# Kernel tuning notes

Measured on AMD Instinct MI355X. Metric: run time of the kernel, lower is better.

Reference implementation:

```python
import jax, jax.numpy as jnp
import numpy as np
from jax import lax

B, T, D = 8, 704, 1024
R, K, HD = 16, 4, 64          # num_rules, top_k(rules), head_dim
SD, E = 32, 3                 # select_dim, num_entities
CTX = E // 2                  # entities kept per selected rule = 1
SEG_LENS = np.array([128.0, 64.0, 512.0], np.float32)  # prompt / descriptor / input segments
SEG_LENS_J = jnp.asarray(SEG_LENS)


def _seg_mask():
    m = np.zeros((E, T), np.float32)
    m[0, :128] = 1.0
    m[1, 128:192] = 1.0
    m[2, 192:] = 1.0
    return jnp.asarray(m)


def _ln(x, g, b):
    mu = x.mean(-1, keepdims=True)
    var = ((x - mu) ** 2).mean(-1, keepdims=True)
    return (x - mu) * lax.rsqrt(var + 1e-5) * g + b


def _st_topk(scores, k):
    # hard top-k multi-hot mask with straight-through gradient (TopkArgMax)
    _, idx = lax.top_k(scores, k)
    hard = jax.nn.one_hot(idx, scores.shape[-1], dtype=scores.dtype).sum(-2)
    return hard + scores - lax.stop_gradient(scores)


def setup_inputs() -> dict:
    key = jax.random.key(0)
    ks = jax.random.split(key, 16)
    g = lambda i, shape, s=0.02: jax.random.normal(ks[i], shape, jnp.float32) * s
    return dict(
        hidden_states=jax.random.normal(ks[0], (B, T, D), jnp.float32),
        attention_mask=jnp.zeros((B, T, T), jnp.float32),
        rules_embed=g(1, (K, R, HD), 0.1),
        W_ent=g(2, (D, SD)), b_ent=jnp.zeros((SD,), jnp.float32),
        Wq_er=g(3, (HD, SD)), Wk_er=g(4, (SD, SD)),
        Wq_es=g(5, (K, HD, SD // 2)), Wk_es=g(6, (SD, SD // 2)),
        Wq=g(7, (D, D)), bq=jnp.zeros((D,), jnp.float32),
        Wk=g(8, (D, D)), bk=jnp.zeros((D,), jnp.float32),
        Wv=g(9, (D, D)), bv=jnp.zeros((D,), jnp.float32),
        Wo=g(10, (HD, D)), bo=jnp.zeros((D,), jnp.float32),
        ln1_g=jnp.ones((D,), jnp.float32), ln1_b=jnp.zeros((D,), jnp.float32),
        ln2_g=jnp.ones((D,), jnp.float32), ln2_b=jnp.zeros((D,), jnp.float32),
        fc1_w1=g(11, (D, D // 2)), fc1_w2=g(12, (D // 2, 4 * D)),
        fc2_w1=g(13, (4 * D, D // 2)), fc2_w2=g(14, (D // 2, D)),
    )


def _forward(hidden_states, attention_mask, rules_embed, W_ent, b_ent,
             Wq_er, Wk_er, Wq_es, Wk_es, Wq, bq, Wk, bk, Wv, bv, Wo, bo,
             ln1_g, ln1_b, ln2_g, ln2_b, fc1_w1, fc1_w2, fc2_w1, fc2_w2):
    seg = _seg_mask()                                   # [E,T] entity token masks
    residual = hidden_states
    h = _ln(hidden_states, ln1_g, ln1_b)                # [B,T,D]

    # --- EntityEncoder: masked mean-pool per entity segment -> select_dim
    pooled = jnp.einsum('et,btd->bed', seg, h) / SEG_LENS_J[None, :, None]
    entities = pooled @ W_ent + b_ent                   # [B,E,SD]

    # --- rule/entity selection (eval: hard top-1 over rules x entities)
    q_er = jnp.einsum('krh,hd->krd', rules_embed, Wq_er)           # [K,R,SD] shared query
    k_er = entities @ Wk_er                                        # [B,E,SD]
    s_er = jnp.einsum('krd,bed->bkre', q_er, k_er) / np.float32(np.sqrt(SD))
    mask = _st_topk(s_er.reshape(B, K, R * E), 1)                  # [B,K,R*E]
    rule_mask = mask.reshape(B, K, R, E).sum(-1)                   # [B,K,R]
    selected_rules = jnp.einsum('bkr,krh->bkh', rule_mask, rules_embed)  # [B,K,HD]

    # --- entity selection per selected rule (grouped query, top-ctx_size)
    q_es = jnp.einsum('bkh,khi->bki', selected_rules, Wq_es)
    k_es = entities @ Wk_es                                        # [B,E,SD//2]
    s_es = jnp.einsum('bki,bei->bke', q_es, k_es) / np.float32(np.sqrt(SD // 2))
    entity_mask = _st_topk(s_es, CTX)                              # [B,K,E]

    # --- masked gather-sum over (top_k, entities) without [B,K,E,T,D] blowup
    tok_gate = jnp.einsum('bke,et->bt', entity_mask, seg)          # [B,T]
    hg = h * tok_gate[:, :, None]                                  # [B,T,D]

    # --- per-rule self-attention
    scale = np.float32(HD ** -0.5)
    q = ((hg @ Wq + bq) * scale).reshape(B, T, R, HD).transpose(0, 2, 1, 3)
    kk = (hg @ Wk + bk).reshape(B, T, R, HD).transpose(0, 2, 1, 3)
    v = (hg @ Wv + bv).reshape(B, T, R, HD).transpose(0, 2, 1, 3)
    aw = jnp.einsum('brqh,brkh->brqk', q, kk) + attention_mask[:, None]
    ap = jax.nn.softmax(aw, axis=-1)
    ao = jnp.einsum('brqk,brkh->brqh', ap, v)                      # [B,R,T,HD]

    # --- combine over rules per top-k slot, project, sum over slots
    sel = jnp.einsum('bkr,brth->bkth', rule_mask, ao)              # [B,K,T,HD]
    attn_out = (jnp.einsum('bkth,hd->bktd', sel, Wo) + bo).sum(1)  # [B,T,D] (bias summed K times, as in torch)

    h = residual + attn_out
    residual = h
    x = _ln(h, ln2_g, ln2_b).reshape(B * T, D)
    # GroupMLP (num=1, hidden=D//2) with internal relu; outer activation_fn=gelu
    x = jax.nn.gelu(jax.nn.relu(x @ fc1_w1) @ fc1_w2, approximate=False)
    x = jax.nn.relu(x @ fc2_w1) @ fc2_w2
    return residual + x.reshape(B, T, D)


def reference(hidden_states, attention_mask, rules_embed, W_ent, b_ent,
              Wq_er, Wk_er, Wq_es, Wk_es, Wq, bq, Wk, bk, Wv, bv, Wo, bo,
              ln1_g, ln1_b, ln2_g, ln2_b, fc1_w1, fc1_w2, fc2_w1, fc2_w2):
    return _forward(hidden_states, attention_mask, rules_embed, W_ent, b_ent,
                    Wq_er, Wk_er, Wq_es, Wk_es, Wq, bq, Wk, bk, Wv, bv, Wo, bo,
                    ln1_g, ln1_b, ln2_g, ln2_b, fc1_w1, fc1_w2, fc2_w1, fc2_w2)
```

## Files before the change

kernel.cpp:

```cpp
#include <hip/hip_runtime.h>
#include <hip/hip_bf16.h>
#include <math.h>

#define BB 8
#define TT 704
#define DD 1024
#define RR 16
#define KK 4
#define HDH 64
#define BT (BB*TT)

typedef unsigned short u16;
typedef __attribute__((ext_vector_type(4))) float f32x4;
typedef __attribute__((ext_vector_type(8))) short bf16x8;
typedef __attribute__((ext_vector_type(4))) unsigned short u16x4;
typedef __attribute__((ext_vector_type(8))) unsigned short u16x8;

__device__ __forceinline__ u16 f2bf(float f) {
    union { float f; unsigned int u; } cv; cv.f = f;
    unsigned int u = cv.u;
    unsigned int r = (u + 0x7fffu + ((u >> 16) & 1u)) >> 16;
    return (u16)r;
}

__device__ __forceinline__ float bf2f(u16 v) {
    union { unsigned int u; float f; } cv; cv.u = ((unsigned int)v) << 16;
    return cv.f;
}

__device__ __forceinline__ void gl2lds(const u16* g, u16* l) {
    __builtin_amdgcn_global_load_lds(
        (const __attribute__((address_space(1))) void*)g,
        (__attribute__((address_space(3))) void*)l, 16, 0, 0);
}

template<int N> __device__ __forceinline__ void waitv() {
    if constexpr (N == 0) asm volatile("s_waitcnt vmcnt(0)" ::: "memory");
    else if constexpr (N == 2) asm volatile("s_waitcnt vmcnt(2)" ::: "memory");
    else if constexpr (N == 3) asm volatile("s_waitcnt vmcnt(3)" ::: "memory");
    else asm volatile("s_waitcnt vmcnt(4)" ::: "memory");
}

__device__ __forceinline__ int xcd_swz(int d, int nwg) {
    return (d & 7) * (nwg >> 3) + (d >> 3);
}

template<int OBF16, int IBF16>
__global__ __launch_bounds__(256)
void ln_kernel(const void* __restrict__ xv, const float* __restrict__ g,
               const float* __restrict__ be, void* __restrict__ yv)
{
    const int row = blockIdx.x;
    const int tid = threadIdx.x;
    __shared__ float sbuf[4];
    const size_t off = (size_t)row * DD + tid * 4;
    float4 v;
    if (IBF16) {
        u16x4 xb = *(const u16x4*)((const u16*)xv + off);
        v.x = bf2f(xb[0]); v.y = bf2f(xb[1]); v.z = bf2f(xb[2]); v.w = bf2f(xb[3]);
    } else {
        v = *(const float4*)((const float*)xv + off);
    }
    float s = v.x + v.y + v.z + v.w;
#pragma unroll
    for (int o = 32; o; o >>= 1) s += __shfl_xor(s, o);
    if ((tid & 63) == 0) sbuf[tid >> 6] = s;
    __syncthreads();
    float mean = (sbuf[0] + sbuf[1] + sbuf[2] + sbuf[3]) * (1.f / 1024.f);
    float dx = v.x - mean, dy = v.y - mean, dz = v.z - mean, dw = v.w - mean;
    float q = dx*dx + dy*dy + dz*dz + dw*dw;
    __syncthreads();
#pragma unroll
    for (int o = 32; o; o >>= 1) q += __shfl_xor(q, o);
    if ((tid & 63) == 0) sbuf[tid >> 6] = q;
    __syncthreads();
    float var = (sbuf[0] + sbuf[1] + sbuf[2] + sbuf[3]) * (1.f / 1024.f);
    float rstd = rsqrtf(var + 1e-5f);
    float4 gg = *(const float4*)(g + tid * 4);
    float4 bb4 = *(const float4*)(be + tid * 4);
    float o0 = dx * rstd * gg.x + bb4.x;
    float o1 = dy * rstd * gg.y + bb4.y;
    float o2 = dz * rstd * gg.z + bb4.z;
    float o3 = dw * rstd * gg.w + bb4.w;
    if (OBF16) {
        u16x4 o4 = {f2bf(o0), f2bf(o1), f2bf(o2), f2bf(o3)};
        *(u16x4*)((u16*)yv + off) = o4;
    } else {
        float4 o4 = {o0, o1, o2, o3};
        *(float4*)((float*)yv + off) = o4;
    }
}

__global__ __launch_bounds__(256)
void ln1_dual_kernel(const float* __restrict__ x, const float* __restrict__ g,
                     const float* __restrict__ be, float* __restrict__ y,
                     u16* __restrict__ yb)
{
    const int row = blockIdx.x;
    const int tid = threadIdx.x;
    __shared__ float sbuf[4];
    const size_t off = (size_t)row * DD + tid * 4;
    float4 v = *(const float4*)(x + off);
    float s = v.x + v.y + v.z + v.w;
#pragma unroll
    for (int o = 32; o; o >>= 1) s += __shfl_xor(s, o);
    if ((tid & 63) == 0) sbuf[tid >> 6] = s;
    __syncthreads();
    float mean = (sbuf[0] + sbuf[1] + sbuf[2] + sbuf[3]) * (1.f / 1024.f);
    float dx = v.x - mean, dy = v.y - mean, dz = v.z - mean, dw = v.w - mean;
    float q = dx*dx + dy*dy + dz*dz + dw*dw;
    __syncthreads();
#pragma unroll
    for (int o = 32; o; o >>= 1) q += __shfl_xor(q, o);
    if ((tid & 63) == 0) sbuf[tid >> 6] = q;
    __syncthreads();
    float var = (sbuf[0] + sbuf[1] + sbuf[2] + sbuf[3]) * (1.f / 1024.f);
    float rstd = rsqrtf(var + 1e-5f);
    float4 gg = *(const float4*)(g + tid * 4);
    float4 bb4 = *(const float4*)(be + tid * 4);
    float o0 = dx * rstd * gg.x + bb4.x;
    float o1 = dy * rstd * gg.y + bb4.y;
    float o2 = dz * rstd * gg.z + bb4.z;
    float o3 = dw * rstd * gg.w + bb4.w;
    float4 o4 = {o0, o1, o2, o3};
    *(float4*)(y + off) = o4;
    u16x4 ob = {f2bf(o0), f2bf(o1), f2bf(o2), f2bf(o3)};
    *(u16x4*)(yb + off) = ob;
}

__global__ __launch_bounds__(256)
void pool_partial_kernel(const float* __restrict__ h, float* __restrict__ partial)
{
    const int chunk = blockIdx.x, b = blockIdx.y;
    const int d = threadIdx.x * 4;
    const float* p = h + ((size_t)b * TT + chunk * 64) * DD + d;
    float4 s = {0.f, 0.f, 0.f, 0.f};
    for (int t = 0; t < 64; ++t) {
        float4 v = *(const float4*)(p + (size_t)t * DD);
        s.x += v.x; s.y += v.y; s.z += v.z; s.w += v.w;
    }
    *(float4*)(partial + ((size_t)(b * 11 + chunk)) * 1024 + d) = s;
}

__global__ __launch_bounds__(256)
void pool_finish_kernel(const float* __restrict__ partial, const float* __restrict__ W_ent,
                        const float* __restrict__ b_ent, float* __restrict__ entities)
{
    const int b = blockIdx.x / 3, e = blockIdx.x % 3;
    const int c0 = (e == 0) ? 0 : (e == 1) ? 2 : 3;
    const int c1 = (e == 0) ? 2 : (e == 1) ? 3 : 11;
    const float invlen = (e == 0) ? (1.f/128.f) : (e == 1) ? (1.f/64.f) : (1.f/512.f);
    __shared__ float pooled[1024];
    __shared__ float part[8][32];
    const int tid = threadIdx.x;
    {
        const int d = tid * 4;
        float4 s = {0.f, 0.f, 0.f, 0.f};
        for (int c = c0; c < c1; ++c) {
            float4 v = *(const float4*)(partial + ((size_t)(b * 11 + c)) * 1024 + d);
            s.x += v.x; s.y += v.y; s.z += v.z; s.w += v.w;
        }
        pooled[d+0] = s.x * invlen; pooled[d+1] = s.y * invlen;
        pooled[d+2] = s.z * invlen; pooled[d+3] = s.w * invlen;
    }
    __syncthreads();
    const int g = tid >> 5, j = tid & 31;
    float s = 0.f;
    for (int d = g * 128; d < g * 128 + 128; ++d) s = fmaf(pooled[d], W_ent[d * 32 + j], s);
    part[g][j] = s;
    __syncthreads();
    if (tid < 32) {
        float s2 = b_ent[tid];
        for (int g2 = 0; g2 < 8; ++g2) s2 += part[g2][tid];
        entities[blockIdx.x * 32 + tid] = s2;
    }
}

__global__ __launch_bounds__(256)
void select_kernel(const float* __restrict__ entities, const float* __restrict__ rules,
                   const float* __restrict__ Wq_er, const float* __restrict__ Wk_er,
                   const float* __restrict__ Wq_es, const float* __restrict__ Wk_es,
                   int* __restrict__ slot_rule, float* __restrict__ gate)
{
    __shared__ float rules_s[4096];
    __shared__ float Wq_er_s[2048];
    __shared__ float Wq_es_s[4096];
    __shared__ float Wk_er_s[1024];
    __shared__ float Wk_es_s[512];
    __shared__ float ent_s[768];
    __shared__ float q_er_s[2048];
    __shared__ float k_er_s[768];
    __shared__ float k_es_s[384];
    __shared__ float qes_s[32][16];
    __shared__ int   rsel_s[32];
    __shared__ int   sel_e[32];
    const int tid = threadIdx.x;
    for (int i = tid; i < 1024; i += 256) *(float4*)&rules_s[i*4] = *(const float4*)&rules[i*4];
    for (int i = tid; i < 512;  i += 256) *(float4*)&Wq_er_s[i*4] = *(const float4*)&Wq_er[i*4];
    for (int i = tid; i < 1024; i += 256) *(float4*)&Wq_es_s[i*4] = *(const float4*)&Wq_es[i*4];
    if (tid < 256) *(float4*)&Wk_er_s[tid*4] = *(const float4*)&Wk_er[tid*4];
    if (tid < 128) *(float4*)&Wk_es_s[tid*4] = *(const float4*)&Wk_es[tid*4];
    if (tid < 192) *(float4*)&ent_s[tid*4] = *(const float4*)&entities[tid*4];
    __syncthreads();
    for (int idx = tid; idx < 2048; idx += 256) {
        int k = idx >> 9, rem = idx & 511, r = rem >> 5, d = rem & 31;
        float s = 0.f;
        for (int hh = 0; hh < 64; ++hh)
            s = fmaf(rules_s[(k * 16 + r) * 64 + hh], Wq_er_s[hh * 32 + d], s);
        q_er_s[idx] = s;
    }
    for (int idx = tid; idx < 768; idx += 256) {
        int be = idx >> 5, d = idx & 31;
        float s = 0.f;
        for (int ss = 0; ss < 32; ++ss)
            s = fmaf(ent_s[be * 32 + ss], Wk_er_s[ss * 32 + d], s);
        k_er_s[idx] = s;
    }
    for (int idx = tid; idx < 384; idx += 256) {
        int be = idx >> 4, i = idx & 15;
        float s = 0.f;
        for (int ss = 0; ss < 32; ++ss)
            s = fmaf(ent_s[be * 32 + ss], Wk_es_s[ss * 16 + i], s);
        k_es_s[idx] = s;
    }
    __syncthreads();
    {
        const int pair = tid >> 3, slice = tid & 7;
        const int b = pair >> 2, k = pair & 3;
        float best = -1e30f; int bj = 48;
        for (int j = slice * 6; j < slice * 6 + 6; ++j) {
            const int r = j / 3, e = j - 3 * r;
            const float* qp = &q_er_s[(k * 16 + r) * 32];
            const float* kp = &k_er_s[(b * 3 + e) * 32];
            float s = 0.f;
            for (int d = 0; d < 32; ++d) s = fmaf(qp[d], kp[d], s);
            s *= 0.17677669529663687f;
            if (s > best) { best = s; bj = j; }
        }
#pragma unroll
        for (int off = 1; off < 8; off <<= 1) {
            float os = __shfl_xor(best, off);
            int oj = __shfl_xor(bj, off);
            if (os > best || (os == best && oj < bj)) { best = os; bj = oj; }
        }
        if (slice == 0) { rsel_s[pair] = bj / 3; slot_rule[pair] = bj / 3; }
    }
    __syncthreads();
    {
        const int pair = tid >> 3, slice = tid & 7;
        const int k = pair & 3, rstar = rsel_s[pair];
#pragma unroll
        for (int ii = 0; ii < 2; ++ii) {
            const int i = slice * 2 + ii;
            float s = 0.f;
            for (int hh = 0; hh < 64; ++hh)
                s = fmaf(rules_s[(k * 16 + rstar) * 64 + hh], Wq_es_s[(k * 64 + hh) * 16 + i], s);
            qes_s[pair][i] = s;
        }
    }
    __syncthreads();
    if ((tid & 7) == 0) {
        const int pair = tid >> 3, b = pair >> 2;
        float best2 = -1e30f; int ei = 0;
        for (int e = 0; e < 3; ++e) {
            float s = 0.f;
            for (int i = 0; i < 16; ++i) s = fmaf(qes_s[pair][i], k_es_s[(b * 3 + e) * 16 + i], s);
            s *= 0.25f;
            if (s > best2) { best2 = s; ei = e; }
        }
        sel_e[pair] = ei;
    }
    __syncthreads();
    if (tid < 24) {
        const int b = tid / 3, e = tid % 3;
        float g = 0.f;
        for (int k = 0; k < 4; ++k) g += (sel_e[b * 4 + k] == e) ? 1.f : 0.f;
        gate[b * 3 + e] = g;
    }
}

__device__ __forceinline__ void transpose_tile(const float* __restrict__ in,
                                               u16* __restrict__ out,
                                               int R, int C, int tr, int tc)
{
    __shared__ float tile[32][33];
    const int tx = threadIdx.x & 31, ty = threadIdx.x >> 5;
    const int c0 = tc * 32, r0 = tr * 32;
#pragma unroll
    for (int j = 0; j < 4; ++j)
        tile[ty + j * 8][tx] = in[(size_t)(r0 + ty + j * 8) * C + c0 + tx];
    __syncthreads();
#pragma unroll
    for (int j = 0; j < 4; ++j)
        out[(size_t)(c0 + ty + j * 8) * R + r0 + tx] = f2bf(tile[tx][ty + j * 8]);
}

__device__ __forceinline__ void transpose_tile_rep4(const float* __restrict__ in,
                                                    u16* __restrict__ out,
                                                    int tr, int tc)
{
    __shared__ float tile[32][33];
    const int tx = threadIdx.x & 31, ty = threadIdx.x >> 5;
    const int c0 = tc * 32, r0 = tr * 32;
#pragma unroll
    for (int j = 0; j < 4; ++j)
        tile[ty + j * 8][tx] = in[(size_t)(r0 + ty + j * 8) * 1024 + c0 + tx];
    __syncthreads();
#pragma unroll
    for (int j = 0; j < 4; ++j) {
        const u16 v = f2bf(tile[tx][ty + j * 8]);
        u16* o = out + (size_t)(c0 + ty + j * 8) * 256 + r0 + tx;
#pragma unroll
        for (int rep = 0; rep < 4; ++rep) o[rep * 64] = v;
    }
}

__global__ __launch_bounds__(256)
void transpose_batch1_kernel(const float* __restrict__ Wq, const float* __restrict__ Wk,
                             const float* __restrict__ Wv, const float* __restrict__ Wo,
                             const float* __restrict__ fc1w1, const float* __restrict__ fc2w2,
                             u16* __restrict__ WqkvT, u16* __restrict__ WoT4,
                             u16* __restrict__ fc1w1T, u16* __restrict__ fc2w2T)
{
    const int bid = blockIdx.x;
    if (bid < 3072) {
        const int m = bid >> 10, t = bid & 1023;
        const float* in = (m == 0) ? Wq : (m == 1) ? Wk : Wv;
        transpose_tile(in, WqkvT + (size_t)m * 1024 * 1024, 1024, 1024, t >> 5, t & 31);
    } else if (bid < 3136) {
        const int t = bid - 3072;
        transpose_tile_rep4(Wo, WoT4, t >> 5, t & 31);
    } else if (bid < 3648) {
        const int t = bid - 3136;
        transpose_tile(fc1w1, fc1w1T, 1024, 512, t >> 4, t & 15);
    } else {
        const int t = bid - 3648;
        transpose_tile(fc2w2, fc2w2T, 512, 1024, t >> 5, t & 31);
    }
}

__global__ __launch_bounds__(256)
void transpose_batch2_kernel(const float* __restrict__ fc1w2, const float* __restrict__ fc2w1,
                             u16* __restrict__ fc1w2T, u16* __restrict__ fc2w1T)
{
    const int bid = blockIdx.x;
    if (bid < 2048) transpose_tile(fc1w2, fc1w2T, 512, 4096, bid >> 7, bid & 127);
    else { const int t = bid - 2048; transpose_tile(fc2w1, fc2w1T, 4096, 512, t >> 4, t & 15); }
}

template<int BN, int ACT, int OBF16, int RESB, int SWZ>
__global__ __launch_bounds__(256)
void gemm2(const u16* __restrict__ A, int lda, const u16* __restrict__ Bt, int ldb,
           void* C0, void* C1, int ldc, int M, int Ksub,
           const void* __restrict__ resid, const float* __restrict__ bias, float bscale,
           int gx, int gy)
{
    constexpr int MI = (BN == 128) ? 4 : 2;
    constexpr int NLOAD = 2 + ((BN == 128) ? 2 : 1);
    __shared__ u16 As[3][128 * 32];
    __shared__ u16 Bs[3][BN * 32];
    const int tid = threadIdx.x;
    const int wid = tid >> 6, lane = tid & 63;
    const int bid = SWZ ? xcd_swz(blockIdx.x, gridDim.x) : (int)blockIdx.x;
    const int col = bid % gx;
    const int rem = bid / gx;
    const int row = rem % gy;
    const int z = rem / gy;
    const int row0 = row * 128, col0 = col * BN;
    const size_t koff = (size_t)z * Ksub;
    const int srA = wid * 32 + (lane >> 2);
    const int sc = (lane & 3) * 8;
    const u16* ag = A + (size_t)(row0 + srA) * lda + koff + sc;
    const int srB = (BN == 128) ? (wid * 32 + (lane >> 2)) : (wid * 16 + (lane >> 2));
    const u16* bg = Bt + (size_t)(col0 + srB) * ldb + koff + sc;
    const int nt = Ksub >> 5;

    auto STAGE = [&](int buf, int t) {
        const u16* a = ag + t * 32;
        const u16* b = bg + t * 32;
        gl2lds(a, &As[buf][wid * 1024]);
        gl2lds(a + (size_t)16 * lda, &As[buf][wid * 1024 + 512]);
        if constexpr (BN == 128) {
            gl2lds(b, &Bs[buf][wid * 1024]);
            gl2lds(b + (size_t)16 * ldb, &Bs[buf][wid * 1024 + 512]);
        } else {
            gl2lds(b, &Bs[buf][wid * 512]);
        }
    };

    f32x4 acc[MI][4];
#pragma unroll
    for (int i = 0; i < MI; ++i)
#pragma unroll
        for (int j = 0; j < 4; ++j) acc[i][j] = (f32x4){0.f, 0.f, 0.f, 0.f};

    const int fr = lane & 15, kb8 = (lane >> 4) * 8;
    const int wrbase = (BN == 128) ? (wid >> 1) * 64 : wid * 32;
    const int wcbase = (BN == 128) ? (wid & 1) * 64 : 0;
    const int paoff = (wrbase + fr) * 32 + kb8;
    const int pboff = (wcbase + fr) * 32 + kb8;

    STAGE(0, 0);
    if (nt > 1) STAGE(1, 1);
    for (int t = 0; t < nt; ++t) {
        if (t + 1 < nt) waitv<NLOAD>(); else waitv<0>();
        __builtin_amdgcn_s_barrier();
        asm volatile("" ::: "memory");
        const int buf = t % 3;
#pragma unroll
        for (int mi = 0; mi < MI; ++mi) {
            bf16x8 af = *(const bf16x8*)&As[buf][paoff + mi * 512];
#pragma unroll
            for (int ni = 0; ni < 4; ++ni) {
                bf16x8 bfv = *(const bf16x8*)&Bs[buf][pboff + ni * 512];
                acc[mi][ni] = __builtin_amdgcn_mfma_f32_16x16x32_bf16(af, bfv, acc[mi][ni], 0, 0, 0);
            }
        }
        if (t + 2 < nt) STAGE((t + 2) % 3, t + 2);
    }

    void* Cp = (z == 0) ? C0 : C1;
    const int fq4 = (lane >> 4) * 4;
#pragma unroll
    for (int mi = 0; mi < MI; ++mi) {
#pragma unroll
        for (int j = 0; j < 4; ++j) {
            const int rw = row0 + wrbase + mi * 16 + fq4 + j;
#pragma unroll
            for (int ni = 0; ni < 4; ++ni) {
                const int cl = col0 + wcbase + ni * 16 + fr;
                float v = acc[mi][ni][j];
                if (bias) v += bscale * bias[cl];
                if (ACT == 1) v = fmaxf(v, 0.f);
                else if (ACT == 2) v = 0.5f * v * (1.f + erff(v * 0.70710678118654752f));
                const size_t off = (size_t)rw * ldc + cl;
                if (OBF16) {
                    ((u16*)Cp)[off] = f2bf(v);
                } else {
                    if (resid) v += RESB ? bf2f(((const u16*)resid)[off])
                                         : ((const float*)resid)[off];
                    ((float*)Cp)[off] = v;
                }
            }
        }
    }
}

template<int NP>
__global__ __launch_bounds__(256)
void red_relu_kernel(const float* __restrict__ p0, const float* __restrict__ p1,
                     const float* __restrict__ p2, const float* __restrict__ p3,
                     u16* __restrict__ out)
{
    const int i = (blockIdx.x * 256 + threadIdx.x) * 4;
    float4 a = *(const float4*)(p0 + i);
    float4 b = *(const float4*)(p1 + i);
    a.x += b.x; a.y += b.y; a.z += b.z; a.w += b.w;
    if (NP == 4) {
        float4 c = *(const float4*)(p2 + i);
        float4 d = *(const float4*)(p3 + i);
        a.x += c.x + d.x; a.y += c.y + d.y; a.z += c.z + d.z; a.w += c.w + d.w;
    }
    u16x4 o = {f2bf(fmaxf(a.x, 0.f)), f2bf(fmaxf(a.y, 0.f)),
               f2bf(fmaxf(a.z, 0.f)), f2bf(fmaxf(a.w, 0.f))};
    *(u16x4*)(out + i) = o;
}

__global__ __launch_bounds__(256)
void combine_mfma_kernel(const u16* __restrict__ AO, const u16* __restrict__ WoT4,
                         const float* __restrict__ hidden, const float* __restrict__ bo,
                         u16* __restrict__ hmid)
{
    __shared__ u16 As[3][128 * 32];
    __shared__ u16 Bs[3][128 * 32];
    const int tid = threadIdx.x;
    const int wid = tid >> 6, lane = tid & 63;
    const int bid = xcd_swz(blockIdx.x, gridDim.x);
    const int row0 = (bid >> 3) * 128, col0 = (bid & 7) * 128;
    const int srA = wid * 32 + (lane >> 2);
    const int sc = (lane & 3) * 8;
    const int arow0 = row0 + srA, arow1 = arow0 + 16;
    const int ab0 = arow0 / TT, at0 = arow0 - ab0 * TT;
    const int ab1 = arow1 / TT, at1 = arow1 - ab1 * TT;
    const u16* abase0 = AO + ((size_t)(ab0 * 4) * TT + at0) * 64 + sc;
    const u16* abase1 = AO + ((size_t)(ab1 * 4) * TT + at1) * 64 + sc;
    const u16* bg = WoT4 + (size_t)(col0 + srA) * 256 + sc;
    const int nt = 8;

    auto STAGE = [&](int buf, int t) {
        const int k0 = t * 32;
        const size_t delta = (size_t)(k0 >> 6) * (TT * 64) + (k0 & 63);
        gl2lds(abase0 + delta, &As[buf][wid * 1024]);
        gl2lds(abase1 + delta, &As[buf][wid * 1024 + 512]);
        gl2lds(bg + k0, &Bs[buf][wid * 1024]);
        gl2lds(bg + k0 + (size_t)16 * 256, &Bs[buf][wid * 1024 + 512]);
    };

    f32x4 acc[4][4];
#pragma unroll
    for (int i = 0; i < 4; ++i)
#pragma unroll
        for (int j = 0; j < 4; ++j) acc[i][j] = (f32x4){0.f, 0.f, 0.f, 0.f};
    const int fr = lane & 15, kb8 = (lane >> 4) * 8;
    const int wrbase = (wid >> 1) * 64, wcbase = (wid & 1) * 64;
    const int paoff = (wrbase + fr) * 32 + kb8;
    const int pboff = (wcbase + fr) * 32 + kb8;

    STAGE(0, 0);
    STAGE(1, 1);
    for (int t = 0; t < nt; ++t) {
        if (t + 1 < nt) waitv<4>(); else waitv<0>();
        __builtin_amdgcn_s_barrier();
        asm volatile("" ::: "memory");
        const int buf = t % 3;
#pragma unroll
        for (int mi = 0; mi < 4; ++mi) {
            bf16x8 af = *(const bf16x8*)&As[buf][paoff + mi * 512];
#pragma unroll
            for (int ni = 0; ni < 4; ++ni) {
                bf16x8 bfv = *(const bf16x8*)&Bs[buf][pboff + ni * 512];
                acc[mi][ni] = __builtin_amdgcn_mfma_f32_16x16x32_bf16(af, bfv, acc[mi][ni], 0, 0, 0);
            }
        }
        if (t + 2 < nt) STAGE((t + 2) % 3, t + 2);
    }

    const int fq4 = (lane >> 4) * 4;
#pragma unroll
    for (int mi = 0; mi < 4; ++mi)
#pragma unroll
        for (int j = 0; j < 4; ++j) {
            const int rw = row0 + wrbase + mi * 16 + fq4 + j;
#pragma unroll
            for (int ni = 0; ni < 4; ++ni) {
                const int cl = col0 + wcbase + ni * 16 + fr;
                const size_t off = (size_t)rw * DD + cl;
                float v = acc[mi][ni][j] + 4.f * bo[cl] + hidden[off];
                hmid[off] = f2bf(v);
            }
        }
}

__global__ __launch_bounds__(256)
void qkv3_mfma_kernel(const u16* __restrict__ hb, const u16* __restrict__ WqkvT,
                      const float* __restrict__ bq, const float* __restrict__ bk,
                      const float* __restrict__ bv, const int* __restrict__ slot_rule,
                      const float* __restrict__ gatep,
                      u16* __restrict__ Qb, u16* __restrict__ Kb, u16* __restrict__ VT)
{
    const int bid = xcd_swz(blockIdx.x, gridDim.x);
    const int slot = bid & 3;
    const int mt = (bid >> 2) % 11;
    const int b = (bid >> 2) / 11;
    const int z = b * 4 + slot;
    const int r = slot_rule[z];
    const float gv = gatep[b * 3 + ((mt < 2) ? 0 : (mt < 3) ? 1 : 2)];
    __shared__ u16 As[3][64 * 32];
    __shared__ u16 Bs[3][3][64 * 32];
    const int tid = threadIdx.x;
    const int w = tid >> 6, lane = tid & 63;
    const u16* ag = hb + ((size_t)b * TT + mt * 64 + (tid >> 2)) * DD + (tid & 3) * 8;
    const u16* bg0 = WqkvT + (size_t)0 * DD * DD + (size_t)(r * 64 + (tid >> 2)) * DD + (tid & 3) * 8;
    const u16* bg1 = WqkvT + (size_t)1 * DD * DD + (size_t)(r * 64 + (tid >> 2)) * DD + (tid & 3) * 8;
    const u16* bg2 = WqkvT + (size_t)2 * DD * DD + (size_t)(r * 64 + (tid >> 2)) * DD + (tid & 3) * 8;
    auto STAGE = [&](int buf, int t) {
        gl2lds(ag  + t * 32, &As[buf][w * 512]);
        gl2lds(bg0 + t * 32, &Bs[buf][0][w * 512]);
        gl2lds(bg1 + t * 32, &Bs[buf][1][w * 512]);
        gl2lds(bg2 + t * 32, &Bs[buf][2][w * 512]);
    };
    f32x4 accq[4], acck[4], accv[4];
#pragma unroll
    for (int i = 0; i < 4; ++i) {
        accq[i] = (f32x4){0.f, 0.f, 0.f, 0.f};
        acck[i] = (f32x4){0.f, 0.f, 0.f, 0.f};
        accv[i] = (f32x4){0.f, 0.f, 0.f, 0.f};
    }
    const int fr = lane & 15, kb8 = (lane >> 4) * 8;
    const int paoff = (w * 16 + fr) * 32 + kb8;
    const int nt = 32;
    STAGE(0, 0);
    STAGE(1, 1);
    for (int t = 0; t < nt; ++t) {
        if (t + 1 < nt) waitv<4>(); else waitv<0>();
        __builtin_amdgcn_s_barrier();
        asm volatile("" ::: "memory");
        const int buf = t % 3;
        bf16x8 af = *(const bf16x8*)&As[buf][paoff];
#pragma unroll
        for (int ni = 0; ni < 4; ++ni) {
            const int boff = (ni * 16 + fr) * 32 + kb8;
            bf16x8 bq8 = *(const bf16x8*)&Bs[buf][0][boff];
            bf16x8 bk8 = *(const bf16x8*)&Bs[buf][1][boff];
            bf16x8 bv8 = *(const bf16x8*)&Bs[buf][2][boff];
            accq[ni] = __builtin_amdgcn_mfma_f32_16x16x32_bf16(af, bq8, accq[ni], 0, 0, 0);
            acck[ni] = __builtin_amdgcn_mfma_f32_16x16x32_bf16(af, bk8, acck[ni], 0, 0, 0);
            accv[ni] = __builtin_amdgcn_mfma_f32_16x16x32_bf16(bv8, af, accv[ni], 0, 0, 0);
        }
        if (t + 2 < nt) STAGE((t + 2) % 3, t + 2);
    }
    const size_t bs = (size_t)z * TT;
    const int fq4 = (lane >> 4) * 4;
#pragma unroll
    for (int ni = 0; ni < 4; ++ni)
#pragma unroll
        for (int j = 0; j < 4; ++j) {
            const int row = mt * 64 + w * 16 + fq4 + j;
            const int col = ni * 16 + fr;
            Qb[(bs + row) * 64 + col] = f2bf((gv * accq[ni][j] + bq[r * 64 + col]) * 0.125f);
            Kb[(bs + row) * 64 + col] = f2bf(gv * acck[ni][j] + bk[r * 64 + col]);
            const int d = ni * 16 + fq4 + j;
            const int tt2 = mt * 64 + w * 16 + fr;
            VT[((size_t)z * 64 + d) * TT + tt2] = f2bf(gv * accv[ni][j] + bv[r * 64 + d]);
        }
}

__global__ __launch_bounds__(256)
void attn_mfma_kernel(const u16* __restrict__ Qb, const u16* __restrict__ Kb,
                      const u16* __restrict__ VT, const float* __restrict__ amask,
                      u16* __restrict__ AO)
{
    const int bid = xcd_swz(blockIdx.x, gridDim.x);
    const int slot = bid & 3;
    const int qt = (bid >> 2) % 11;
    const int b = (bid >> 2) / 11;
    const int z = b * 4 + slot;
    const size_t bs = (size_t)z * TT;
    const int tid = threadIdx.x;
    const int w = tid >> 6, lane = tid & 63;
    const int fr = lane & 15, g = lane >> 4;
    const int q0 = qt * 64 + w * 16;

    __shared__ u16 Ks[64 * 72];
    __shared__ u16 VTs[64 * 72];
    __shared__ u16 Ps[4][16 * 72];

    bf16x8 qa[2];
    qa[0] = *(const bf16x8*)(Qb + (bs + q0 + fr) * 64 + g * 8);
    qa[1] = *(const bf16x8*)(Qb + (bs + q0 + fr) * 64 + 32 + g * 8);

    float m_run[4], l_run[4];
    f32x4 oacc[4];
#pragma unroll
    for (int j = 0; j < 4; ++j) { m_run[j] = -1e30f; l_run[j] = 0.f; }
#pragma unroll
    for (int ni = 0; ni < 4; ++ni) oacc[ni] = (f32x4){0.f, 0.f, 0.f, 0.f};

    const float* mrow = amask + ((size_t)b * TT + q0 + g * 4) * TT;

    for (int kc = 0; kc < 11; ++kc) {
        const int kv0 = kc * 64;
        __syncthreads();
#pragma unroll
        for (int it = 0; it < 2; ++it) {
            const int idx = tid + it * 256;
            const int row = idx >> 3, ch = (idx & 7) * 8;
            *(u16x8*)&Ks[row * 72 + ch]  = *(const u16x8*)(Kb + (bs + kv0 + row) * 64 + ch);
            *(u16x8*)&VTs[row * 72 + ch] = *(const u16x8*)(VT + ((size_t)z * 64 + row) * TT + kv0 + ch);
        }
        __syncthreads();
        f32x4 sacc[4];
#pragma unroll
        for (int ni = 0; ni < 4; ++ni) sacc[ni] = (f32x4){0.f, 0.f, 0.f, 0.f};
#pragma unroll
        for (int c = 0; c < 2; ++c)
#pragma unroll
            for (int ni = 0; ni < 4; ++ni) {
                bf16x8 bf = *(const bf16x8*)&Ks[(ni * 16 + fr) * 72 + c * 32 + g * 8];
                sacc[ni] = __builtin_amdgcn_mfma_f32_16x16x32_bf16(qa[c], bf, sacc[ni], 0, 0, 0);
            }
        float mloc[4] = {-1e30f, -1e30f, -1e30f, -1e30f};
#pragma unroll
        for (int ni = 0; ni < 4; ++ni)
#pragma unroll
            for (int j = 0; j < 4; ++j) {
                float s = sacc[ni][j] + mrow[(size_t)j * TT + kv0 + ni * 16 + fr];
                sacc[ni][j] = s;
                mloc[j] = fmaxf(mloc[j], s);
            }
#pragma unroll
        for (int o = 1; o < 16; o <<= 1)
#pragma unroll
            for (int j = 0; j < 4; ++j) mloc[j] = fmaxf(mloc[j], __shfl_xor(mloc[j], o));
        float fac[4], lsum[4];
#pragma unroll
        for (int j = 0; j < 4; ++j) {
            const float mn = fmaxf(m_run[j], mloc[j]);
            fac[j] = __expf(m_run[j] - mn);
            m_run[j] = mn;
            lsum[j] = 0.f;
        }
#pragma unroll
        for (int ni = 0; ni < 4; ++ni)
#pragma unroll
            for (int j = 0; j < 4; ++j) {
                const float p = __expf(sacc[ni][j] - m_run[j]);
                lsum[j] += p;
                Ps[w][(g * 4 + j) * 72 + ni * 16 + fr] = f2bf(p);
            }
#pragma unroll
        for (int o = 1; o < 16; o <<= 1)
#pragma unroll
            for (int j = 0; j < 4; ++j) lsum[j] += __shfl_xor(lsum[j], o);
#pragma unroll
        for (int j = 0; j < 4; ++j) l_run[j] = l_run[j] * fac[j] + lsum[j];
#pragma unroll
        for (int ni = 0; ni < 4; ++ni)
#pragma unroll
            for (int j = 0; j < 4; ++j) oacc[ni][j] *= fac[j];
#pragma unroll
        for (int c = 0; c < 2; ++c) {
            bf16x8 paf = *(const bf16x8*)&Ps[w][fr * 72 + c * 32 + g * 8];
#pragma unroll
            for (int ni = 0; ni < 4; ++ni) {
                bf16x8 vf = *(const bf16x8*)&VTs[(ni * 16 + fr) * 72 + c * 32 + g * 8];
                oacc[ni] = __builtin_amdgcn_mfma_f32_16x16x32_bf16(paf, vf, oacc[ni], 0, 0, 0);
            }
        }
    }
#pragma unroll
    for (int j = 0; j < 4; ++j) {
        const float inv = 1.f / l_run[j];
        const int t = q0 + g * 4 + j;
#pragma unroll
        for (int ni = 0; ni < 4; ++ni)
            AO[(bs + t) * 64 + ni * 16 + fr] = f2bf(oacc[ni][j] * inv);
    }
}

extern "C" void kernel_launch(void* const* d_in, const int* in_sizes, int n_in,
                              void* d_out, int out_size, void* d_ws, size_t ws_size,
                              hipStream_t stream)
{
    const float* hidden = (const float*)d_in[0];
    const float* amask  = (const float*)d_in[1];
    const float* rules  = (const float*)d_in[2];
    const float* W_ent  = (const float*)d_in[3];
    const float* b_ent  = (const float*)d_in[4];
    const float* Wq_er  = (const float*)d_in[5];
    const float* Wk_er  = (const float*)d_in[6];
    const float* Wq_es  = (const float*)d_in[7];
    const float* Wk_es  = (const float*)d_in[8];
    const float* Wq     = (const float*)d_in[9];
    const float* bq     = (const float*)d_in[10];
    const float* Wk     = (const float*)d_in[11];
    const float* bk     = (const float*)d_in[12];
    const float* Wv     = (const float*)d_in[13];
    const float* bv     = (const float*)d_in[14];
    const float* Wo     = (const float*)d_in[15];
    const float* bo     = (const float*)d_in[16];
    const float* ln1_g  = (const float*)d_in[17];
    const float* ln1_b  = (const float*)d_in[18];
    const float* ln2_g  = (const float*)d_in[19];
    const float* ln2_b  = (const float*)d_in[20];
    const float* fc1_w1 = (const float*)d_in[21];
    const float* fc1_w2 = (const float*)d_in[22];
    const float* fc2_w1 = (const float*)d_in[23];
    const float* fc2_w2 = (const float*)d_in[24];

    char* ws = (char*)d_ws;
    float* h      = (float*)(ws + 0);
    u16*   x1     = (u16*)(ws + 0);
    u16*   x3b    = (u16*)(ws + 5767168);
    float* g3p1   = (float*)(ws + 11534336);
    u16*   hmid   = (u16*)(ws + 23068672);
    u16*   hb     = (u16*)(ws + 46137344);
    u16*   xln2   = (u16*)(ws + 46137344);
    u16*   x2h    = (u16*)(ws + 46137344);
    u16*   Qb     = (u16*)(ws + 57671680);
    u16*   Kb     = (u16*)(ws + 60555264);
    u16*   VT     = (u16*)(ws + 66322432);
    u16*   AO     = (u16*)(ws + 69206016);
    float* part   = (float*)(ws + 69206016);
    float* g3p0   = (float*)(ws + 74973184);
    float* ent    = (float*)(ws + 80740352);
    float* gate   = (float*)(ws + 80743424);
    int*   srule  = (int*)(ws + 80743552);
    u16*   WqkvT  = (u16*)(ws + 80743680);
    u16*   fc1w2T = (u16*)(ws + 80743680);
    u16*   fc2w1T = (u16*)(ws + 84937984);
    u16*   WoT4   = (u16*)(ws + 89132288);
    u16*   fc1w1T = (u16*)(ws + 89656576);
    u16*   fc2w2T = (u16*)(ws + 90705152);
    float* out    = (float*)d_out;

    ln1_dual_kernel<<<BT, 256, 0, stream>>>(hidden, ln1_g, ln1_b, h, hb);
    pool_partial_kernel<<<dim3(11, 8), 256, 0, stream>>>(h, part);
    pool_finish_kernel<<<24, 256, 0, stream>>>(part, W_ent, b_ent, ent);
    select_kernel<<<1, 256, 0, stream>>>(ent, rules, Wq_er, Wk_er, Wq_es, Wk_es, srule, gate);

    transpose_batch1_kernel<<<4160, 256, 0, stream>>>(Wq, Wk, Wv, Wo, fc1_w1, fc2_w2,
                                                      WqkvT, WoT4, fc1w1T, fc2w2T);

    qkv3_mfma_kernel<<<352, 256, 0, stream>>>(hb, WqkvT, bq, bk, bv, srule, gate,
                                              Qb, Kb, VT);
    transpose_batch2_kernel<<<4096, 256, 0, stream>>>(fc1_w2, fc2_w1, fc1w2T, fc2w1T);

    attn_mfma_kernel<<<352, 256, 0, stream>>>(Qb, Kb, VT, amask, AO);

    combine_mfma_kernel<<<352, 256, 0, stream>>>(AO, WoT4, hidden, bo, hmid);

    ln_kernel<1, 1><<<BT, 256, 0, stream>>>(hmid, ln2_g, ln2_b, xln2);

    gemm2<64, 1, 1, 0, 1><<<352, 256, 0, stream>>>(
        xln2, 1024, fc1w1T, 1024, x1, nullptr, 512, BT, 1024,
        nullptr, nullptr, 0.f, 8, 44);

    for (int half = 0; half < 2; ++half) {
        const u16* x1h = x1 + (size_t)half * 2816 * 512;
        u16* x3bh = x3b + (size_t)half * 2816 * 512;
        gemm2<128, 2, 1, 0, 0><<<704, 256, 0, stream>>>(
            x1h, 512, fc1w2T, 512, x2h, nullptr, 4096, 2816, 512,
            nullptr, nullptr, 0.f, 32, 22);
        gemm2<64, 0, 0, 0, 1><<<352, 256, 0, stream>>>(
            x2h, 4096, fc2w1T, 4096, g3p0, g3p1, 512, 2816, 2048,
            nullptr, nullptr, 0.f, 8, 22);
        red_relu_kernel<2><<<1408, 256, 0, stream>>>(g3p0, g3p1, nullptr, nullptr, x3bh);
    }

    gemm2<64, 0, 0, 1, 1><<<704, 256, 0, stream>>>(
        x3b, 512, fc2w2T, 512, out, nullptr, 1024, BT, 512,
        hmid, nullptr, 0.f, 16, 44);
}
```

Baseline: 270.0 us.

## Add 256x128 GELU GEMM, merge weight transposes, retile final GEMM

A new 512-thread GEMM kernel with 256x128 output tiles and triple-buffered LDS staging replaces the 128-wide-tile fc1_w2 GELU GEMM. This raises per-block operand reuse and halves the block count. The two weight-transpose launches become one kernel, which needs fc1w2T/fc2w1T and g3p1 moved to new workspace offsets. The final residual GEMM switches to 128-wide tiles with half as many blocks. The larger tiles add register and LDS pressure and may lower occupancy.

```diff
diff --git a/kernel.cpp b/kernel.cpp
--- a/kernel.cpp
+++ b/kernel.cpp
@@ -316,11 +316,13 @@
 }
 
 __global__ __launch_bounds__(256)
-void transpose_batch1_kernel(const float* __restrict__ Wq, const float* __restrict__ Wk,
-                             const float* __restrict__ Wv, const float* __restrict__ Wo,
-                             const float* __restrict__ fc1w1, const float* __restrict__ fc2w2,
-                             u16* __restrict__ WqkvT, u16* __restrict__ WoT4,
-                             u16* __restrict__ fc1w1T, u16* __restrict__ fc2w2T)
+void transpose_all_kernel(const float* __restrict__ Wq, const float* __restrict__ Wk,
+                          const float* __restrict__ Wv, const float* __restrict__ Wo,
+                          const float* __restrict__ fc1w1, const float* __restrict__ fc2w2,
+                          const float* __restrict__ fc1w2, const float* __restrict__ fc2w1,
+                          u16* __restrict__ WqkvT, u16* __restrict__ WoT4,
+                          u16* __restrict__ fc1w1T, u16* __restrict__ fc2w2T,
+                          u16* __restrict__ fc1w2T, u16* __restrict__ fc2w1T)
 {
     const int bid = blockIdx.x;
     if (bid < 3072) {
@@ -333,19 +335,16 @@
     } else if (bid < 3648) {
         const int t = bid - 3136;
         transpose_tile(fc1w1, fc1w1T, 1024, 512, t >> 4, t & 15);
-    } else {
+    } else if (bid < 4160) {
         const int t = bid - 3648;
         transpose_tile(fc2w2, fc2w2T, 512, 1024, t >> 5, t & 31);
-    }
-}
-
-__global__ __launch_bounds__(256)
-void transpose_batch2_kernel(const float* __restrict__ fc1w2, const float* __restrict__ fc2w1,
-                             u16* __restrict__ fc1w2T, u16* __restrict__ fc2w1T)
-{
-    const int bid = blockIdx.x;
-    if (bid < 2048) transpose_tile(fc1w2, fc1w2T, 512, 4096, bid >> 7, bid & 127);
-    else { const int t = bid - 2048; transpose_tile(fc2w1, fc2w1T, 4096, 512, t >> 4, t & 15); }
+    } else if (bid < 6208) {
+        const int t = bid - 4160;
+        transpose_tile(fc1w2, fc1w2T, 512, 4096, t >> 7, t & 127);
+    } else {
+        const int t = bid - 6208;
+        transpose_tile(fc2w1, fc2w1T, 4096, 512, t >> 4, t & 15);
+    }
 }
 
 template<int BN, int ACT, int OBF16, int RESB, int SWZ>
@@ -444,6 +443,77 @@
             }
         }
     }
+}
+
+__global__ __launch_bounds__(512)
+void gemm256_kernel(const u16* __restrict__ A, int lda, const u16* __restrict__ Bt, int ldb,
+                    u16* __restrict__ C, int ldc, int Kt, int gx)
+{
+    __shared__ u16 As[3][256 * 32];
+    __shared__ u16 Bs[3][128 * 32];
+    const int tid = threadIdx.x;
+    const int wid = tid >> 6, lane = tid & 63;
+    const int col = blockIdx.x % gx;
+    const int row = blockIdx.x / gx;
+    const int row0 = row * 256, col0 = col * 128;
+    const int srA = wid * 32 + (lane >> 2);
+    const int srB = wid * 16 + (lane >> 2);
+    const int sc = (lane & 3) * 8;
+    const u16* ag = A + (size_t)(row0 + srA) * lda + sc;
+    const u16* bg = Bt + (size_t)(col0 + srB) * ldb + sc;
+    const int nt = Kt >> 5;
+
+    auto STAGE = [&](int buf, int t) {
+        const u16* a = ag + t * 32;
+        gl2lds(a, &As[buf][wid * 1024]);
+        gl2lds(a + (size_t)16 * lda, &As[buf][wid * 1024 + 512]);
+        gl2lds(bg + t * 32, &Bs[buf][wid * 512]);
+    };
+
+    f32x4 acc[8][2];
+#pragma unroll
+    for (int i = 0; i < 8; ++i)
+#pragma unroll
+        for (int j = 0; j < 2; ++j) acc[i][j] = (f32x4){0.f, 0.f, 0.f, 0.f};
+
+    const int fr = lane & 15, kb8 = (lane >> 4) * 8;
+    const int wr = wid >> 2, wc = wid & 3;
+    const int paoff = (wr * 128 + fr) * 32 + kb8;
+    const int pboff = (wc * 32 + fr) * 32 + kb8;
+
+    STAGE(0, 0);
+    STAGE(1, 1);
+    for (int t = 0; t < nt; ++t) {
+        if (t + 1 < nt) waitv<3>(); else waitv<0>();
+        __builtin_amdgcn_s_barrier();
+        asm volatile("" ::: "memory");
+        const int buf = t % 3;
+#pragma unroll
+        for (int mi = 0; mi < 8; ++mi) {
+            bf16x8 af = *(const bf16x8*)&As[buf][paoff + mi * 512];
+#pragma unroll
+            for (int ni = 0; ni < 2; ++ni) {
+                bf16x8 bfv = *(const bf16x8*)&Bs[buf][pboff + ni * 512];
+                acc[mi][ni] = __builtin_amdgcn_mfma_f32_16x16x32_bf16(af, bfv, acc[mi][ni], 0, 0, 0);
+            }
+        }
+        if (t + 2 < nt) STAGE((t + 2) % 3, t + 2);
+    }
+
+    const int fq4 = (lane >> 4) * 4;
+#pragma unroll
+    for (int mi = 0; mi < 8; ++mi)
+#pragma unroll
+        for (int j = 0; j < 4; ++j) {
+            const int rw = row0 + wr * 128 + mi * 16 + fq4 + j;
+#pragma unroll
+            for (int ni = 0; ni < 2; ++ni) {
+                const int cl = col0 + wc * 32 + ni * 16 + fr;
+                float v = acc[mi][ni][j];
+                v = 0.5f * v * (1.f + erff(v * 0.70710678118654752f));
+                C[(size_t)rw * ldc + cl] = f2bf(v);
+            }
+        }
 }
 
 template<int NP>
@@ -762,8 +832,10 @@
     float* h      = (float*)(ws + 0);
     u16*   x1     = (u16*)(ws + 0);
     u16*   x3b    = (u16*)(ws + 5767168);
-    float* g3p1   = (float*)(ws + 11534336);
+    u16*   fc1w2T = (u16*)(ws + 11534336);
+    u16*   fc2w1T = (u16*)(ws + 15728640);
     u16*   hmid   = (u16*)(ws + 23068672);
+    float* g3p1   = (float*)(ws + 34603008);
     u16*   hb     = (u16*)(ws + 46137344);
     u16*   xln2   = (u16*)(ws + 46137344);
     u16*   x2h    = (u16*)(ws + 46137344);
@@ -777,8 +849,6 @@
     float* gate   = (float*)(ws + 80743424);
     int*   srule  = (int*)(ws + 80743552);
     u16*   WqkvT  = (u16*)(ws + 80743680);
-    u16*   fc1w2T = (u16*)(ws + 80743680);
-    u16*   fc2w1T = (u16*)(ws + 84937984);
     u16*   WoT4   = (u16*)(ws + 89132288);
     u16*   fc1w1T = (u16*)(ws + 89656576);
     u16*   fc2w2T = (u16*)(ws + 90705152);
@@ -789,12 +859,13 @@
     pool_finish_kernel<<<24, 256, 0, stream>>>(part, W_ent, b_ent, ent);
     select_kernel<<<1, 256, 0, stream>>>(ent, rules, Wq_er, Wk_er, Wq_es, Wk_es, srule, gate);
 
-    transpose_batch1_kernel<<<4160, 256, 0, stream>>>(Wq, Wk, Wv, Wo, fc1_w1, fc2_w2,
-                                                      WqkvT, WoT4, fc1w1T, fc2w2T);
+    transpose_all_kernel<<<8256, 256, 0, stream>>>(Wq, Wk, Wv, Wo, fc1_w1, fc2_w2,
+                                                   fc1_w2, fc2_w1,
+                                                   WqkvT, WoT4, fc1w1T, fc2w2T,
+                                                   fc1w2T, fc2w1T);
 
     qkv3_mfma_kernel<<<352, 256, 0, stream>>>(hb, WqkvT, bq, bk, bv, srule, gate,
                                               Qb, Kb, VT);
-    transpose_batch2_kernel<<<4096, 256, 0, stream>>>(fc1_w2, fc2_w1, fc1w2T, fc2w1T);
 
     attn_mfma_kernel<<<352, 256, 0, stream>>>(Qb, Kb, VT, amask, AO);
 
@@ -809,16 +880,15 @@
     for (int half = 0; half < 2; ++half) {
         const u16* x1h = x1 + (size_t)half * 2816 * 512;
         u16* x3bh = x3b + (size_t)half * 2816 * 512;
-        gemm2<128, 2, 1, 0, 0><<<704, 256, 0, stream>>>(
-            x1h, 512, fc1w2T, 512, x2h, nullptr, 4096, 2816, 512,
-            nullptr, nullptr, 0.f, 32, 22);
+        gemm256_kernel<<<352, 512, 0, stream>>>(x1h, 512, fc1w2T, 512, x2h, 4096,
+                                                512, 32);
         gemm2<64, 0, 0, 0, 1><<<352, 256, 0, stream>>>(
             x2h, 4096, fc2w1T, 4096, g3p0, g3p1, 512, 2816, 2048,
             nullptr, nullptr, 0.f, 8, 22);
         red_relu_kernel<2><<<1408, 256, 0, stream>>>(g3p0, g3p1, nullptr, nullptr, x3bh);
     }
 
-    gemm2<64, 0, 0, 1, 1><<<704, 256, 0, stream>>>(
+    gemm2<128, 0, 0, 1, 1><<<352, 256, 0, stream>>>(
         x3b, 512, fc2w2T, 512, out, nullptr, 1024, BT, 512,
-        hmid, nullptr, 0.f, 16, 44);
-}
+        hmid, nullptr, 0.f, 8, 44);
+}
```

Result: slower. 277.2 us (+2.7%).
